# Kernel optimization log

Measured on AMD Instinct MI355X. Metric: run time of the kernel, lower is better.

## Reference

```python
import jax, jax.numpy as jnp
import numpy as np
import math

B, S, D, H = 2, 1024, 1024, 16
HD = D // H
MAX_ITERS = 4
BETA_0, BETA_DELTA = 0.8, 0.2
MOMENTUM = 0.2
FREQ_FACTOR, PHASE_OFFSET = 2.0, 0.0


def setup_inputs() -> dict:
    key = jax.random.key(0)
    ks = jax.random.split(key, 10)
    s = 1.0 / math.sqrt(D)
    return {
        "x": jax.random.normal(ks[0], (B, S, D), dtype=jnp.float32),
        "Wq": jax.random.normal(ks[1], (D, D), dtype=jnp.float32) * s,
        "bq": jnp.zeros((D,), dtype=jnp.float32),
        "Wk": jax.random.normal(ks[2], (D, D), dtype=jnp.float32) * s,
        "bk": jnp.zeros((D,), dtype=jnp.float32),
        "Wv": jax.random.normal(ks[3], (D, D), dtype=jnp.float32) * s,
        "bv": jnp.zeros((D,), dtype=jnp.float32),
        "Wo": jax.random.normal(ks[4], (D, D), dtype=jnp.float32) * s,
        "bo": jnp.zeros((D,), dtype=jnp.float32),
        "resonance_bias": jnp.zeros((1, H, 1, 1), dtype=jnp.float32),
        "phase_factors": jnp.full((1, H, 1, 1), 0.1, dtype=jnp.float32),
    }


def reference(x, Wq, bq, Wk, bk, Wv, bv, Wo, bo, resonance_bias, phase_factors):
    # Projections -> [B, H, S, HD]
    def split_heads(t):
        return t.reshape(B, S, H, HD).transpose(0, 2, 1, 3)

    q = split_heads(x @ Wq.T + bq)
    k = split_heads(x @ Wk.T + bk)
    v = split_heads(x @ Wv.T + bv)

    scale = 1.0 / math.sqrt(HD)
    attn = None
    for t in range(MAX_ITERS):
        # Phase modulation: shift Q/K by learned per-head phase factors
        t_norm = t / MAX_ITERS
        phase = jnp.sin(jnp.float32(FREQ_FACTOR * t_norm * math.pi + PHASE_OFFSET))
        q_mod = q + phase_factors * phase
        k_mod = k + phase_factors * phase
        # Temperature scheduling: inverse temperature grows each iteration
        beta = BETA_0 + BETA_DELTA * t
        scores = beta * scale * jnp.einsum("bhsd,bhtd->bhst", q_mod, k_mod) + resonance_bias
        attn_new = jax.nn.softmax(scores, axis=-1)
        # Momentum-based attention update
        attn = attn_new if attn is None else MOMENTUM * attn + (1.0 - MOMENTUM) * attn_new

    ctx = jnp.einsum("bhst,bhtd->bhsd", attn, v)  # [B,H,S,HD]
    ctx = ctx.transpose(0, 2, 1, 3).reshape(B, S, D)
    return ctx @ Wo.T + bo
```

## Files before the change

### kernel.cpp

```cpp
#include <hip/hip_runtime.h>
#include <hip/hip_bf16.h>
#include <math.h>

#define BB 2
#define SS 1024
#define DD 1024
#define HH 16
#define HD 64
#define BH (BB*HH)

typedef __attribute__((ext_vector_type(8))) short short8_t;
typedef __attribute__((ext_vector_type(4))) float f32x4;

#if __has_builtin(__builtin_amdgcn_exp2f)
#define EXP2(x) __builtin_amdgcn_exp2f(x)
#else
#define EXP2(x) exp2f(x)
#endif

__device__ __forceinline__ ushort f2bf(float f) {
    union { float f; unsigned u; } a; a.f = f;
    unsigned u = a.u;
    u += 0x7FFFu + ((u >> 16) & 1u);
    return (ushort)(u >> 16);
}
__device__ __forceinline__ float bf2f(ushort b) {
    union { unsigned u; float f; } a; a.u = ((unsigned)b) << 16;
    return a.f;
}
__device__ __forceinline__ unsigned pkbf(float a, float b) {
    unsigned r;
    asm("v_cvt_pk_bf16_f32 %0, %1, %2" : "=v"(r) : "v"(a), "v"(b));
    return r;
}

__global__ __launch_bounds__(256) void cvt_all_kernel(
    const float* __restrict__ x,  const float* __restrict__ wq,
    const float* __restrict__ wk, const float* __restrict__ wv,
    const float* __restrict__ wo,
    ushort* __restrict__ xb,  ushort* __restrict__ wqb, ushort* __restrict__ wkb,
    ushort* __restrict__ wvb, ushort* __restrict__ wob)
{
    int bid = blockIdx.x;
    const float* src; ushort* dst; int off;
    if (bid < 2048) { src = x; dst = xb; off = bid; }
    else {
        int seg = (bid - 2048) >> 10;
        off = (bid - 2048) & 1023;
        if (seg == 0)      { src = wq; dst = wqb; }
        else if (seg == 1) { src = wk; dst = wkb; }
        else if (seg == 2) { src = wv; dst = wvb; }
        else               { src = wo; dst = wob; }
    }
    int i = (off * 256 + threadIdx.x) * 4;
    float4 v = *reinterpret_cast<const float4*>(src + i);
    ushort4 o;
    o.x = f2bf(v.x); o.y = f2bf(v.y); o.z = f2bf(v.z); o.w = f2bf(v.w);
    *reinterpret_cast<ushort4*>(dst + i) = o;
}

template<int BM, int BN, int OUT_F32>
__device__ __forceinline__ void gemm_body(
    const ushort* __restrict__ A, const ushort* __restrict__ Bm,
    const float* __restrict__ bias, void* __restrict__ Cout,
    int N, int K, float scale, int omode,
    const float* __restrict__ pf, float* __restrict__ E1, float* __restrict__ E3,
    float a1, float a3)
{
    constexpr int BK = 32;
    __shared__ ushort lsa[BM * BK];
    __shared__ ushort lsb[BN * BK];
    const int tid  = threadIdx.x;
    const int lane = tid & 63;
    const int wave = tid >> 6;
    constexpr int RI = BM / 32;
    constexpr int CI = BN / 32;
    constexpr int ACH = BM / 16;
    constexpr int TCH = ACH + BN / 16;
    const int wrow = (wave >> 1) * (BM / 2);
    const int wcol = (wave & 1) * (BN / 2);
    const int tileM = blockIdx.y * BM;
    const int tileN = blockIdx.x * BN;
    const int fr  = lane & 15;
    const int fks = (lane >> 4) * 8;
    const int l4  = lane >> 2;
    const int lm4 = lane & 3;
    f32x4 acc[RI][CI] = {};

    for (int kb = 0; kb < K; kb += BK) {
        __syncthreads();
        #pragma unroll
        for (int i = 0; i < TCH / 4; ++i) {
            int chunk = wave * (TCH / 4) + i;
            if (chunk < ACH) {
                const ushort* g = A + (size_t)(tileM + chunk * 16 + l4) * K + kb + lm4 * 8;
                __builtin_amdgcn_global_load_lds(
                    (const __attribute__((address_space(1))) unsigned*)g,
                    (__attribute__((address_space(3))) unsigned*)&lsa[chunk * 512], 16, 0, 0);
            } else {
                int bc = chunk - ACH;
                const ushort* g = Bm + (size_t)(tileN + bc * 16 + l4) * K + kb + lm4 * 8;
                __builtin_amdgcn_global_load_lds(
                    (const __attribute__((address_space(1))) unsigned*)g,
                    (__attribute__((address_space(3))) unsigned*)&lsb[bc * 512], 16, 0, 0);
            }
        }
        __syncthreads();
        short8_t af[RI], bfg[CI];
        #pragma unroll
        for (int r = 0; r < RI; ++r)
            af[r] = *reinterpret_cast<const short8_t*>(&lsa[(wrow + r * 16 + fr) * BK + fks]);
        #pragma unroll
        for (int c = 0; c < CI; ++c)
            bfg[c] = *reinterpret_cast<const short8_t*>(&lsb[(wcol + c * 16 + fr) * BK + fks]);
        #pragma unroll
        for (int r = 0; r < RI; ++r)
            #pragma unroll
            for (int c = 0; c < CI; ++c)
                acc[r][c] = __builtin_amdgcn_mfma_f32_16x16x32_bf16(af[r], bfg[c], acc[r][c], 0, 0, 0);
    }

    const int rr = (lane >> 4) * 4;
    #pragma unroll
    for (int r = 0; r < RI; ++r) {
        #pragma unroll
        for (int c = 0; c < CI; ++c) {
            int n = tileN + wcol + c * 16 + fr;
            float bv = bias[n];
            #pragma unroll
            for (int q = 0; q < 4; ++q) {
                int m = tileM + wrow + r * 16 + rr + q;
                float v = (acc[r][c][q] + bv) * scale;
                if (OUT_F32) {
                    ((float*)Cout)[(size_t)m * N + n] = v;
                } else if (omode == 0) {
                    ((ushort*)Cout)[(size_t)m * N + n] = f2bf(v);
                } else {
                    int bh = ((m >> 10) << 4) + (n >> 6);
                    int j  = m & 1023;
                    int d  = n & 63;
                    if (omode == 2)
                        ((ushort*)Cout)[((size_t)bh * 1024 + j) * 64 + d] = f2bf(v);
                    else
                        ((ushort*)Cout)[(((size_t)(bh * 32 + (j >> 5)) * 64 + d)) * 32 + (j & 31)] = f2bf(v);
                }
            }
        }
    }

    if (!OUT_F32 && omode == 2 && CI == 4) {
        int h = ((tileN + wcol) >> 6) & 15;
        float apf1 = a1 * pf[h];
        float apf3 = a3 * pf[h];
        #pragma unroll
        for (int r = 0; r < RI; ++r) {
            #pragma unroll
            for (int q = 0; q < 4; ++q) {
                float s = 0.f;
                #pragma unroll
                for (int c = 0; c < CI; ++c)
                    s += acc[r][c][q] + bias[tileN + wcol + c * 16 + fr];
                s += __shfl_xor(s, 1);
                s += __shfl_xor(s, 2);
                s += __shfl_xor(s, 4);
                s += __shfl_xor(s, 8);
                if (fr == 0) {
                    int m = tileM + wrow + r * 16 + rr + q;
                    int idx = ((m >> 10) * 16 + h) * 1024 + (m & 1023);
                    E1[idx] = __expf(apf1 * s);
                    E3[idx] = __expf(apf3 * s);
                }
            }
        }
    }
}

__global__ __launch_bounds__(256) void gemm_qkv_kernel(
    const ushort* __restrict__ xb,
    const ushort* __restrict__ wq, const ushort* __restrict__ wk, const ushort* __restrict__ wv,
    const float* __restrict__ bq, const float* __restrict__ bk, const float* __restrict__ bv,
    ushort* __restrict__ Qb, ushort* __restrict__ Kh, ushort* __restrict__ Vt2,
    const float* __restrict__ pf, float* __restrict__ E1, float* __restrict__ E3,
    float qscale, float a1, float a3)
{
    const ushort* Bm; const float* bias; ushort* out; float sc; int omode;
    if (blockIdx.z == 0)      { Bm = wq; bias = bq; out = Qb;  sc = qscale; omode = 0; }
    else if (blockIdx.z == 1) { Bm = wk; bias = bk; out = Kh;  sc = 1.0f;   omode = 2; }
    else                      { Bm = wv; bias = bv; out = Vt2; sc = 1.0f;   omode = 3; }
    gemm_body<64, 128, 0>(xb, Bm, bias, out, DD, DD, sc, omode, pf, E1, E3, a1, a3);
}

__global__ __launch_bounds__(256) void gemm_out_kernel(
    const ushort* __restrict__ ctxb, const ushort* __restrict__ wo,
    const float* __restrict__ bo, float* __restrict__ out)
{
    gemm_body<64, 64, 1>(ctxb, wo, bo, out, DD, DD, 1.0f, 0, nullptr, nullptr, nullptr, 0.f, 0.f);
}

__global__ __launch_bounds__(256) void attn_kernel(
    const ushort* __restrict__ Qb, const ushort* __restrict__ Kh,
    const ushort* __restrict__ Vt2, const float* __restrict__ E1,
    const float* __restrict__ E3, ushort* __restrict__ ctxb)
{
    __shared__ ushort ycache[4][32][264];
    __shared__ float lbuf[4][4][32];
    const int wg  = blockIdx.x;
    const int swz = (wg & 7) * 128 + (wg >> 3);
    const int bh  = swz >> 5;
    const int qb  = (swz & 31) * 32;
    const int b = bh >> 4, h = bh & 15;
    const int wave = threadIdx.x >> 6;
    const int lane = threadIdx.x & 63;
    const int fr = lane & 15;
    const int g  = lane >> 4;
    const int fk = g * 8;

    const float wt[4] = {0.008f, 0.032f, 0.16f, 0.8f};

    const ushort* qbase0 = Qb + (size_t)(b * SS + qb + fr) * DD + h * HD;
    const ushort* qbase1 = Qb + (size_t)(b * SS + qb + 16 + fr) * DD + h * HD;
    const short8_t aq0a = *reinterpret_cast<const short8_t*>(qbase0 + fk);
    const short8_t aq1a = *reinterpret_cast<const short8_t*>(qbase0 + 32 + fk);
    const short8_t aq0b = *reinterpret_cast<const short8_t*>(qbase1 + fk);
    const short8_t aq1b = *reinterpret_cast<const short8_t*>(qbase1 + 32 + fk);

    const float* e1h = E1 + bh * SS;
    const float* e3h = E3 + bh * SS;
    const ushort* khead = Kh + (size_t)bh * SS * HD;
    const ushort* vhead = Vt2 + (size_t)bh * (SS / 32) * HD * 32;

    float lA[4][4] = {}, lB[4][4] = {};
    for (int it = 0; it < 4; ++it) {
        const int k0 = wave * 256 + it * 64;
        #pragma unroll
        for (int n = 0; n < 4; ++n) {
            const ushort* kb = khead + (size_t)(k0 + n * 16 + fr) * HD;
            short8_t bk0 = *reinterpret_cast<const short8_t*>(kb + fk);
            short8_t bk1 = *reinterpret_cast<const short8_t*>(kb + 32 + fk);
            f32x4 za = {0.f, 0.f, 0.f, 0.f};
            f32x4 zb = {0.f, 0.f, 0.f, 0.f};
            za = __builtin_amdgcn_mfma_f32_16x16x32_bf16(aq0a, bk0, za, 0, 0, 0);
            za = __builtin_amdgcn_mfma_f32_16x16x32_bf16(aq1a, bk1, za, 0, 0, 0);
            zb = __builtin_amdgcn_mfma_f32_16x16x32_bf16(aq0b, bk0, zb, 0, 0, 0);
            zb = __builtin_amdgcn_mfma_f32_16x16x32_bf16(aq1b, bk1, zb, 0, 0, 0);
            float e1v = e1h[k0 + n * 16 + fr];
            float e3v = e3h[k0 + n * 16 + fr];
            #pragma unroll
            for (int r = 0; r < 4; ++r) {
                float ya  = EXP2(za[r]);
                float ya2 = ya * ya;
                float ya4 = ya2 * ya2;
                float ya6 = ya4 * ya2;
                lA[0][r] += ya4;
                lA[1][r] += ya4 * ya * e1v;
                lA[2][r] += ya6;
                lA[3][r] += ya6 * ya * e3v;
                ycache[wave][g * 4 + r][it * 64 + n * 16 + fr] = f2bf(ya);
                float yb  = EXP2(zb[r]);
                float yb2 = yb * yb;
                float yb4 = yb2 * yb2;
                float yb6 = yb4 * yb2;
                lB[0][r] += yb4;
                lB[1][r] += yb4 * yb * e1v;
                lB[2][r] += yb6;
                lB[3][r] += yb6 * yb * e3v;
                ycache[wave][16 + g * 4 + r][it * 64 + n * 16 + fr] = f2bf(yb);
            }
        }
    }
    #pragma unroll
    for (int t = 0; t < 4; ++t)
        #pragma unroll
        for (int r = 0; r < 4; ++r) {
            float sa = lA[t][r];
            sa += __shfl_xor(sa, 1);
            sa += __shfl_xor(sa, 2);
            sa += __shfl_xor(sa, 4);
            sa += __shfl_xor(sa, 8);
            lA[t][r] = sa;
            float sb = lB[t][r];
            sb += __shfl_xor(sb, 1);
            sb += __shfl_xor(sb, 2);
            sb += __shfl_xor(sb, 4);
            sb += __shfl_xor(sb, 8);
            lB[t][r] = sb;
        }
    if (fr == 0) {
        #pragma unroll
        for (int t = 0; t < 4; ++t)
            #pragma unroll
            for (int r = 0; r < 4; ++r) {
                lbuf[wave][t][g * 4 + r]      = lA[t][r];
                lbuf[wave][t][16 + g * 4 + r] = lB[t][r];
            }
    }
    __syncthreads();

    float wlA[4], wlB[4];
    #pragma unroll
    for (int t = 0; t < 4; ++t) {
        float sa = lbuf[0][t][fr] + lbuf[1][t][fr] + lbuf[2][t][fr] + lbuf[3][t][fr];
        float sb = lbuf[0][t][16 + fr] + lbuf[1][t][16 + fr] + lbuf[2][t][16 + fr] + lbuf[3][t][16 + fr];
        wlA[t] = wt[t] / sa;
        wlB[t] = wt[t] / sb;
    }

    f32x4 caccA[4] = {}, caccB[4] = {};
    union FragU { short8_t s; unsigned u[4]; };
    for (int it = 0; it < 4; ++it) {
        const int k0 = wave * 256 + it * 64;
        #pragma unroll
        for (int half = 0; half < 2; ++half) {
            short8_t ya8 = *reinterpret_cast<const short8_t*>(
                &ycache[wave][fr][it * 64 + half * 32 + fk]);
            short8_t yb8 = *reinterpret_cast<const short8_t*>(
                &ycache[wave][16 + fr][it * 64 + half * 32 + fk]);
            const float* e1p = e1h + k0 + half * 32 + fk;
            const float* e3p = e3h + k0 + half * 32 + fk;
            float4 e1a = *reinterpret_cast<const float4*>(e1p);
            float4 e1b = *reinterpret_cast<const float4*>(e1p + 4);
            float4 e3a = *reinterpret_cast<const float4*>(e3p);
            float4 e3b = *reinterpret_cast<const float4*>(e3p + 4);
            FragU paA, paB;
            #pragma unroll
            for (int i = 0; i < 4; ++i) {
                float pva[2], pvb[2];
                #pragma unroll
                for (int j = 0; j < 2; ++j) {
                    const int e = 2 * i + j;
                    float e1v = (e < 4) ? ((const float*)&e1a)[e] : ((const float*)&e1b)[e - 4];
                    float e3v = (e < 4) ? ((const float*)&e3a)[e] : ((const float*)&e3b)[e - 4];
                    float ya  = bf2f((ushort)ya8[e]);
                    float ya2 = ya * ya;
                    float ya4 = ya2 * ya2;
                    float t1a = fmaf(ya, wlA[1] * e1v, wlA[0]);
                    float t2a = fmaf(ya, wlA[3] * e3v, wlA[2]);
                    pva[j] = ya4 * fmaf(ya2, t2a, t1a);
                    float yb  = bf2f((ushort)yb8[e]);
                    float yb2 = yb * yb;
                    float yb4 = yb2 * yb2;
                    float t1b = fmaf(yb, wlB[1] * e1v, wlB[0]);
                    float t2b = fmaf(yb, wlB[3] * e3v, wlB[2]);
                    pvb[j] = yb4 * fmaf(yb2, t2b, t1b);
                }
                paA.u[i] = pkbf(pva[0], pva[1]);
                paB.u[i] = pkbf(pvb[0], pvb[1]);
            }
            const ushort* vt = vhead + (size_t)((k0 + half * 32) >> 5) * HD * 32;
            #pragma unroll
            for (int n2 = 0; n2 < 4; ++n2) {
                short8_t v = *reinterpret_cast<const short8_t*>(
                    vt + (n2 * 16 + fr) * 32 + fk);
                caccA[n2] = __builtin_amdgcn_mfma_f32_16x16x32_bf16(paA.s, v, caccA[n2], 0, 0, 0);
                caccB[n2] = __builtin_amdgcn_mfma_f32_16x16x32_bf16(paB.s, v, caccB[n2], 0, 0, 0);
            }
        }
    }

    __syncthreads();
    float* ctxp = (float*)&ycache[wave][0][0];
    #pragma unroll
    for (int n2 = 0; n2 < 4; ++n2)
        #pragma unroll
        for (int q = 0; q < 4; ++q) {
            ctxp[(g * 4 + q) * 68 + n2 * 16 + fr]        = caccA[n2][q];
            ctxp[(16 + g * 4 + q) * 68 + n2 * 16 + fr]   = caccB[n2][q];
        }
    __syncthreads();

    const int d0 = (threadIdx.x & 15) * 4;
    float* base = (float*)&ycache[0][0][0];
    #pragma unroll
    for (int rr = 0; rr < 2; ++rr) {
        int row = rr * 16 + (threadIdx.x >> 4);
        float4 s0 = *reinterpret_cast<float4*>(base + 0 * 4224 + row * 68 + d0);
        float4 s1 = *reinterpret_cast<float4*>(base + 1 * 4224 + row * 68 + d0);
        float4 s2 = *reinterpret_cast<float4*>(base + 2 * 4224 + row * 68 + d0);
        float4 s3 = *reinterpret_cast<float4*>(base + 3 * 4224 + row * 68 + d0);
        float ox = s0.x + s1.x + s2.x + s3.x;
        float oy = s0.y + s1.y + s2.y + s3.y;
        float oz = s0.z + s1.z + s2.z + s3.z;
        float ow = s0.w + s1.w + s2.w + s3.w;
        uint2 o;
        o.x = pkbf(ox, oy);
        o.y = pkbf(oz, ow);
        size_t off = (size_t)(b * SS + qb + row) * DD + h * HD + d0;
        *reinterpret_cast<uint2*>(ctxb + off) = o;
    }
}

extern "C" void kernel_launch(void* const* d_in, const int* in_sizes, int n_in,
                              void* d_out, int out_size, void* d_ws, size_t ws_size,
                              hipStream_t stream) {
    const float* x  = (const float*)d_in[0];
    const float* Wq = (const float*)d_in[1];
    const float* bq = (const float*)d_in[2];
    const float* Wk = (const float*)d_in[3];
    const float* bk = (const float*)d_in[4];
    const float* Wv = (const float*)d_in[5];
    const float* bv = (const float*)d_in[6];
    const float* Wo = (const float*)d_in[7];
    const float* bo = (const float*)d_in[8];
    const float* pf = (const float*)d_in[10];

    ushort* xb   = (ushort*)d_ws;
    ushort* wqb  = xb  + (size_t)2 * 1024 * 1024;
    ushort* wkb  = wqb + (size_t)1024 * 1024;
    ushort* wvb  = wkb + (size_t)1024 * 1024;
    ushort* wob  = wvb + (size_t)1024 * 1024;
    ushort* Qb   = wob + (size_t)1024 * 1024;
    ushort* Kh   = Qb  + (size_t)2 * 1024 * 1024;
    ushort* Vt2  = Kh  + (size_t)2 * 1024 * 1024;
    ushort* ctxb = Vt2 + (size_t)2 * 1024 * 1024;
    float*  E1p  = (float*)(ctxb + (size_t)2 * 1024 * 1024);
    float*  E3p  = E1p + (size_t)BH * SS;

    float ph[4], ctv[4];
    for (int t = 0; t < 4; ++t) {
        double tn = (double)t / 4.0;
        ph[t]  = sinf((float)(2.0 * tn * M_PI + 0.0));
        ctv[t] = (float)((0.8 + 0.2 * (double)t) * 0.125);
    }
    const double LOG2E = 1.44269504088896340736;
    float qscale = (float)(0.025 * LOG2E);
    float a1 = ctv[1] * ph[1];
    float a3 = ctv[3] * ph[3];

    cvt_all_kernel<<<6144, 256, 0, stream>>>(x, Wq, Wk, Wv, Wo, xb, wqb, wkb, wvb, wob);

    gemm_qkv_kernel<<<dim3(8, 32, 3), 256, 0, stream>>>(xb, wqb, wkb, wvb, bq, bk, bv,
                                                        Qb, Kh, Vt2, pf, E1p, E3p,
                                                        qscale, a1, a3);

    attn_kernel<<<1024, 256, 0, stream>>>(Qb, Kh, Vt2, E1p, E3p, ctxb);

    gemm_out_kernel<<<dim3(16, 32), 256, 0, stream>>>(ctxb, wob, bo, (float*)d_out);
}
```

Baseline: 99.28 us.

## Fuse Q/K/V projections into one GEMM kernel sharing the x tile

Replaces the three-way blockIdx.z QKV GEMM, which used 64x128 tiles, with one kernel that loads a 64x64 x tile once and computes the Q, K and V outputs from it. Each of the four waves issues direct global-to-LDS loads for one operand. Row sums of K for the E1/E3 phase exponentials are now reduced across waves through shared memory. This removes the repeated reads of x, but it lowers per-block arithmetic intensity per weight and raises accumulator register pressure. The grid goes from 768 blocks to 512.

```diff
diff --git a/kernel.cpp b/kernel.cpp
--- a/kernel.cpp
+++ b/kernel.cpp
@@ -59,13 +59,139 @@
     *reinterpret_cast<ushort4*>(dst + i) = o;
 }
 
-template<int BM, int BN, int OUT_F32>
-__device__ __forceinline__ void gemm_body(
+__global__ __launch_bounds__(256) void gemm_qkv_fused(
+    const ushort* __restrict__ xb,
+    const ushort* __restrict__ wq, const ushort* __restrict__ wk, const ushort* __restrict__ wv,
+    const float* __restrict__ bq, const float* __restrict__ bk, const float* __restrict__ bvp,
+    ushort* __restrict__ Qb, ushort* __restrict__ Kh, ushort* __restrict__ Vt2,
+    const float* __restrict__ pf, float* __restrict__ E1, float* __restrict__ E3,
+    float qscale, float a1, float a3)
+{
+    constexpr int BK = 32;
+    __shared__ ushort lsa[64 * BK];
+    __shared__ ushort lsb[3][64 * BK];
+    __shared__ float rkbuf[2][64];
+    const int tid  = threadIdx.x;
+    const int lane = tid & 63;
+    const int wave = tid >> 6;
+    const int wrow = (wave >> 1) * 32;
+    const int wcol = (wave & 1) * 32;
+    const int tileM = blockIdx.y * 64;
+    const int tileN = blockIdx.x * 64;
+    const int fr  = lane & 15;
+    const int fks = (lane >> 4) * 8;
+    const int l4  = lane >> 2;
+    const int lm4 = lane & 3;
+    f32x4 acc[3][2][2] = {};
+
+    const ushort* src = (wave == 0) ? xb : ((wave == 1) ? wq : ((wave == 2) ? wk : wv));
+    const int srow = (wave == 0) ? tileM : tileN;
+    ushort* ldst = (wave == 0) ? lsa : lsb[wave - 1];
+
+    for (int kb = 0; kb < DD; kb += BK) {
+        __syncthreads();
+        #pragma unroll
+        for (int i = 0; i < 4; ++i) {
+            const ushort* g = src + (size_t)(srow + i * 16 + l4) * DD + kb + lm4 * 8;
+            __builtin_amdgcn_global_load_lds(
+                (const __attribute__((address_space(1))) unsigned*)g,
+                (__attribute__((address_space(3))) unsigned*)&ldst[i * 512], 16, 0, 0);
+        }
+        __syncthreads();
+        short8_t af[2];
+        #pragma unroll
+        for (int r = 0; r < 2; ++r)
+            af[r] = *reinterpret_cast<const short8_t*>(&lsa[(wrow + r * 16 + fr) * BK + fks]);
+        #pragma unroll
+        for (int t = 0; t < 3; ++t) {
+            #pragma unroll
+            for (int c = 0; c < 2; ++c) {
+                short8_t bfg = *reinterpret_cast<const short8_t*>(
+                    &lsb[t][(wcol + c * 16 + fr) * BK + fks]);
+                #pragma unroll
+                for (int r = 0; r < 2; ++r)
+                    acc[t][r][c] = __builtin_amdgcn_mfma_f32_16x16x32_bf16(af[r], bfg, acc[t][r][c], 0, 0, 0);
+            }
+        }
+    }
+
+    const int rr = (lane >> 4) * 4;
+    const int b  = tileM >> 10;
+    const int h  = (tileN >> 6) & 15;
+    const int bh = b * 16 + h;
+
+    #pragma unroll
+    for (int r = 0; r < 2; ++r)
+        #pragma unroll
+        for (int c = 0; c < 2; ++c) {
+            int n = tileN + wcol + c * 16 + fr;
+            float bb = bq[n];
+            #pragma unroll
+            for (int q = 0; q < 4; ++q) {
+                int m = tileM + wrow + r * 16 + rr + q;
+                Qb[(size_t)m * DD + n] = f2bf((acc[0][r][c][q] + bb) * qscale);
+            }
+        }
+
+    float rkp[2][4] = {};
+    #pragma unroll
+    for (int r = 0; r < 2; ++r)
+        #pragma unroll
+        for (int c = 0; c < 2; ++c) {
+            int n = tileN + wcol + c * 16 + fr;
+            float bb = bk[n];
+            int d = n & 63;
+            #pragma unroll
+            for (int q = 0; q < 4; ++q) {
+                int m = tileM + wrow + r * 16 + rr + q;
+                float v = acc[1][r][c][q] + bb;
+                rkp[r][q] += v;
+                Kh[((size_t)bh * 1024 + (m & 1023)) * 64 + d] = f2bf(v);
+            }
+        }
+    #pragma unroll
+    for (int r = 0; r < 2; ++r)
+        #pragma unroll
+        for (int q = 0; q < 4; ++q) {
+            float s = rkp[r][q];
+            s += __shfl_xor(s, 1);
+            s += __shfl_xor(s, 2);
+            s += __shfl_xor(s, 4);
+            s += __shfl_xor(s, 8);
+            if (fr == 0) rkbuf[wave & 1][wrow + r * 16 + rr + q] = s;
+        }
+
+    #pragma unroll
+    for (int r = 0; r < 2; ++r)
+        #pragma unroll
+        for (int c = 0; c < 2; ++c) {
+            int n = tileN + wcol + c * 16 + fr;
+            float bb = bvp[n];
+            int d = n & 63;
+            #pragma unroll
+            for (int q = 0; q < 4; ++q) {
+                int m = tileM + wrow + r * 16 + rr + q;
+                int j = m & 1023;
+                Vt2[((size_t)(bh * 32 + (j >> 5)) * 64 + d) * 32 + (j & 31)] =
+                    f2bf(acc[2][r][c][q] + bb);
+            }
+        }
+
+    __syncthreads();
+    if (tid < 64) {
+        float rk = rkbuf[0][tid] + rkbuf[1][tid];
+        int m = tileM + tid;
+        int idx = bh * 1024 + (m & 1023);
+        float p = pf[h];
+        E1[idx] = __expf(a1 * p * rk);
+        E3[idx] = __expf(a3 * p * rk);
+    }
+}
+
+template<int BM, int BN>
+__device__ __forceinline__ void gemm_out_body(
     const ushort* __restrict__ A, const ushort* __restrict__ Bm,
-    const float* __restrict__ bias, void* __restrict__ Cout,
-    int N, int K, float scale, int omode,
-    const float* __restrict__ pf, float* __restrict__ E1, float* __restrict__ E3,
-    float a1, float a3)
+    const float* __restrict__ bias, float* __restrict__ Cout, int N, int K)
 {
     constexpr int BK = 32;
     __shared__ ushort lsa[BM * BK];
@@ -122,79 +248,24 @@
 
     const int rr = (lane >> 4) * 4;
     #pragma unroll
-    for (int r = 0; r < RI; ++r) {
+    for (int r = 0; r < RI; ++r)
         #pragma unroll
         for (int c = 0; c < CI; ++c) {
             int n = tileN + wcol + c * 16 + fr;
-            float bv = bias[n];
+            float bb = bias[n];
             #pragma unroll
             for (int q = 0; q < 4; ++q) {
                 int m = tileM + wrow + r * 16 + rr + q;
-                float v = (acc[r][c][q] + bv) * scale;
-                if (OUT_F32) {
-                    ((float*)Cout)[(size_t)m * N + n] = v;
-                } else if (omode == 0) {
-                    ((ushort*)Cout)[(size_t)m * N + n] = f2bf(v);
-                } else {
-                    int bh = ((m >> 10) << 4) + (n >> 6);
-                    int j  = m & 1023;
-                    int d  = n & 63;
-                    if (omode == 2)
-                        ((ushort*)Cout)[((size_t)bh * 1024 + j) * 64 + d] = f2bf(v);
-                    else
-                        ((ushort*)Cout)[(((size_t)(bh * 32 + (j >> 5)) * 64 + d)) * 32 + (j & 31)] = f2bf(v);
-                }
-            }
-        }
-    }
-
-    if (!OUT_F32 && omode == 2 && CI == 4) {
-        int h = ((tileN + wcol) >> 6) & 15;
-        float apf1 = a1 * pf[h];
-        float apf3 = a3 * pf[h];
-        #pragma unroll
-        for (int r = 0; r < RI; ++r) {
-            #pragma unroll
-            for (int q = 0; q < 4; ++q) {
-                float s = 0.f;
-                #pragma unroll
-                for (int c = 0; c < CI; ++c)
-                    s += acc[r][c][q] + bias[tileN + wcol + c * 16 + fr];
-                s += __shfl_xor(s, 1);
-                s += __shfl_xor(s, 2);
-                s += __shfl_xor(s, 4);
-                s += __shfl_xor(s, 8);
-                if (fr == 0) {
-                    int m = tileM + wrow + r * 16 + rr + q;
-                    int idx = ((m >> 10) * 16 + h) * 1024 + (m & 1023);
-                    E1[idx] = __expf(apf1 * s);
-                    E3[idx] = __expf(apf3 * s);
-                }
-            }
-        }
-    }
-}
-
-__global__ __launch_bounds__(256) void gemm_qkv_kernel(
-    const ushort* __restrict__ xb,
-    const ushort* __restrict__ wq, const ushort* __restrict__ wk, const ushort* __restrict__ wv,
-    const float* __restrict__ bq, const float* __restrict__ bk, const float* __restrict__ bv,
-    ushort* __restrict__ Qb, ushort* __restrict__ Kh, ushort* __restrict__ Vt2,
-    const float* __restrict__ pf, float* __restrict__ E1, float* __restrict__ E3,
-    float qscale, float a1, float a3)
-{
-    const ushort* Bm; const float* bias; ushort* out; float sc; int omode;
-    if (blockIdx.z == 0)      { Bm = wq; bias = bq; out = Qb;  sc = qscale; omode = 0; }
-    else if (blockIdx.z == 1) { Bm = wk; bias = bk; out = Kh;  sc = 1.0f;   omode = 2; }
-    else                      { Bm = wv; bias = bv; out = Vt2; sc = 1.0f;   omode = 3; }
-    gemm_body<64, 128, 0>(xb, Bm, bias, out, DD, DD, sc, omode, pf, E1, E3, a1, a3);
+                Cout[(size_t)m * N + n] = acc[r][c][q] + bb;
+            }
+        }
 }
 
 __global__ __launch_bounds__(256) void gemm_out_kernel(
     const ushort* __restrict__ ctxb, const ushort* __restrict__ wo,
     const float* __restrict__ bo, float* __restrict__ out)
 {
-    gemm_body<64, 64, 1>(ctxb, wo, bo, out, DD, DD, 1.0f, 0, nullptr, nullptr, nullptr, 0.f, 0.f);
+    gemm_out_body<64, 64>(ctxb, wo, bo, out, DD, DD);
 }
 
 __global__ __launch_bounds__(256) void attn_kernel(
@@ -428,9 +499,9 @@
 
     cvt_all_kernel<<<6144, 256, 0, stream>>>(x, Wq, Wk, Wv, Wo, xb, wqb, wkb, wvb, wob);
 
-    gemm_qkv_kernel<<<dim3(8, 32, 3), 256, 0, stream>>>(xb, wqb, wkb, wvb, bq, bk, bv,
-                                                        Qb, Kh, Vt2, pf, E1p, E3p,
-                                                        qscale, a1, a3);
+    gemm_qkv_fused<<<dim3(16, 32), 256, 0, stream>>>(xb, wqb, wkb, wvb, bq, bk, bv,
+                                                     Qb, Kh, Vt2, pf, E1p, E3p,
+                                                     qscale, a1, a3);
 
     attn_kernel<<<1024, 256, 0, stream>>>(Qb, Kh, Vt2, E1p, E3p, ctxb);
 
```

After: 97.71 us, median of 2. No clear change (-1.6%).
